# Performance work log

Measured on AMD Instinct MI355X. Metric: run time of the kernel, lower is better.

Reference implementation:

```python
import jax, jax.numpy as jnp
import numpy as np

# Module config (matches init_kwargs)
IC, OC = 8, 16
KH, KW = 3, 3
H, W = 32, 32
PAD, STRIDE = 1, 1
PH, PW = H + 2 * PAD, W + 2 * PAD          # padded input dims: 34x34
OH = (PH - KH) // STRIDE + 1                # 32
OW = (PW - KW) // STRIDE + 1                # 32
B = 64                                       # batch of flattened ciphertext images


def _build_toeplitz(kernel: np.ndarray) -> np.ndarray:
    """approximate_toeplitz_multiple_channels: dense [OC*OH*OW, IC*PH*PW] matrix
    such that T @ vec(padded_x) == vec(conv2d(x, kernel))."""
    T = np.zeros((OC * OH * OW, IC * PH * PW), dtype=np.float32)
    oh, ow = np.meshgrid(np.arange(OH), np.arange(OW), indexing="ij")
    oh, ow = oh.ravel(), ow.ravel()
    for oc in range(OC):
        rows = (oc * OH + oh) * OW + ow
        for ic in range(IC):
            for kh in range(KH):
                for kw in range(KW):
                    cols = (ic * PH + oh * STRIDE + kh) * PW + (ow * STRIDE + kw)
                    T[rows, cols] = kernel[oc, ic, kh, kw]
    return T


def _build_pad_mat() -> np.ndarray:
    """create_padding_transformation_matrix: [IC*PH*PW, IC*H*W] 0/1 matrix that
    zero-pads the flattened image (homomorphic padding as a matmul)."""
    P = np.zeros((IC * PH * PW, IC * H * W), dtype=np.float32)
    ic, h, w = np.meshgrid(np.arange(IC), np.arange(H), np.arange(W), indexing="ij")
    rows = (ic * PH + h + PAD) * PW + (w + PAD)
    cols = (ic * H + h) * W + w
    P[rows.ravel(), cols.ravel()] = 1.0
    return P


def setup_inputs() -> dict:
    rng = np.random.default_rng(0)
    kernel = rng.standard_normal((OC, IC, KH, KW)).astype(np.float32)
    weight = jnp.asarray(_build_toeplitz(kernel))                 # [OC*OH*OW, IC*PH*PW]
    bias = jnp.asarray(
        np.repeat(rng.standard_normal(OC).astype(np.float32), OH * OW)
    )                                                             # [OC*OH*OW]
    pad_mat = jnp.asarray(_build_pad_mat())                       # [IC*PH*PW, IC*H*W]
    key = jax.random.key(0)
    enc_x = jax.random.normal(key, (B, IC * H * W), dtype=jnp.float32)
    return {"enc_x": enc_x, "weight": weight, "bias": bias, "pad_mat": pad_mat}


def reference(enc_x, weight, bias, pad_mat):
    # Homomorphic conv as plaintext-equivalent math:
    # 1) pad via transformation matrix, 2) Toeplitz matmul, 3) add repeated bias.
    x_padded = enc_x @ pad_mat.T            # [B, IC*PH*PW]
    return x_padded @ weight.T + bias       # [B, OC*OH*OW]
```

## Files before the change

### kernel.cpp

```cpp
#include <hip/hip_runtime.h>

#define IC    8
#define OC    16
#define H     32
#define W     32
#define PH    34
#define PW    34
#define OH    32
#define OW    32
#define BATCH 64
#define WCOLS (IC * PH * PW)
#define XSTR  35
#define PLANE (PH * XSTR)
#define HALO  134

__global__ __launch_bounds__(256, 2) void conv_toeplitz_kernel(
    const float* __restrict__ x,
    const float* __restrict__ weight,
    const float* __restrict__ bias,
    float* __restrict__ out)
{
    __shared__ float wk[2][IC * 9];
    __shared__ float xs[IC * PLANE];

    const int tid = threadIdx.x;
    const int blk = blockIdx.x;
    const int b   = blk >> 3;
    const int oc0 = (blk & 7) << 1;

    if (tid < 144) {
        const int os = tid / 72;
        const int k  = tid - os * 72;
        const int ic = k / 9;
        const int r  = k - ic * 9;
        const int kh = r / 3;
        const int kw = r - kh * 3;
        wk[os][k] = weight[(size_t)((oc0 + os) * OH * OW) * WCOLS
                           + (ic * PH + kh) * PW + kw];
    }

    for (int i = tid; i < IC * HALO; i += 256) {
        const int plane = i / HALO;
        const int r     = i - plane * HALO;
        int row, col;
        if (r < 35)       { row = 0;          col = r;        }
        else if (r < 70)  { row = 33;         col = r - 35;   }
        else if (r < 102) { row = r - 70 + 1; col = 0;        }
        else              { row = r - 102 + 1; col = 33;      }
        xs[plane * PLANE + row * XSTR + col] = 0.0f;
    }

    const float4* xg = (const float4*)(x + (size_t)b * (IC * H * W));
    #pragma unroll
    for (int i = 0; i < 8; ++i) {
        const int k   = tid + i * 256;
        const float4 v = xg[k];
        const int ic  = k >> 8;
        const int rem = k & 255;
        const int h   = rem >> 3;
        const int w4  = (rem & 7) << 2;
        float* dst = &xs[ic * PLANE + (h + 1) * XSTR + (w4 + 1)];
        dst[0] = v.x; dst[1] = v.y; dst[2] = v.z; dst[3] = v.w;
    }
    __syncthreads();

    float wreg[2][IC * 9];
    #pragma unroll
    for (int o = 0; o < 2; ++o)
        #pragma unroll
        for (int k = 0; k < IC * 9; ++k)
            wreg[o][k] = wk[o][k];

    const int oh   = tid >> 3;
    const int ow0  = (tid & 7) << 2;
    const int oidx = oh * OW + ow0;

    const float4 b0 = *(const float4*)(bias + oc0 * OH * OW + oidx);
    const float4 b1 = *(const float4*)(bias + (oc0 + 1) * OH * OW + oidx);
    float a00 = b0.x, a01 = b0.y, a02 = b0.z, a03 = b0.w;
    float a10 = b1.x, a11 = b1.y, a12 = b1.z, a13 = b1.w;

    #pragma unroll
    for (int ic = 0; ic < IC; ++ic) {
        #pragma unroll
        for (int kh = 0; kh < 3; ++kh) {
            const float* row = &xs[ic * PLANE + (oh + kh) * XSTR + ow0];
            const float v0 = row[0], v1 = row[1], v2 = row[2];
            const float v3 = row[3], v4 = row[4], v5 = row[5];
            const float w00 = wreg[0][ic * 9 + kh * 3];
            const float w01 = wreg[0][ic * 9 + kh * 3 + 1];
            const float w02 = wreg[0][ic * 9 + kh * 3 + 2];
            const float w10 = wreg[1][ic * 9 + kh * 3];
            const float w11 = wreg[1][ic * 9 + kh * 3 + 1];
            const float w12 = wreg[1][ic * 9 + kh * 3 + 2];
            a00 += v0 * w00 + v1 * w01 + v2 * w02;
            a01 += v1 * w00 + v2 * w01 + v3 * w02;
            a02 += v2 * w00 + v3 * w01 + v4 * w02;
            a03 += v3 * w00 + v4 * w01 + v5 * w02;
            a10 += v0 * w10 + v1 * w11 + v2 * w12;
            a11 += v1 * w10 + v2 * w11 + v3 * w12;
            a12 += v2 * w10 + v3 * w11 + v4 * w12;
            a13 += v3 * w10 + v4 * w11 + v5 * w12;
        }
    }

    float* o0 = out + (size_t)(b * OC + oc0) * (OH * OW) + oidx;
    *(float4*)o0 = make_float4(a00, a01, a02, a03);
    float* o1 = o0 + OH * OW;
    *(float4*)o1 = make_float4(a10, a11, a12, a13);
}

extern "C" void kernel_launch(void* const* d_in, const int* in_sizes, int n_in,
                              void* d_out, int out_size, void* d_ws, size_t ws_size,
                              hipStream_t stream) {
    const float* x      = (const float*)d_in[0];
    const float* weight = (const float*)d_in[1];
    const float* bias   = (const float*)d_in[2];
    float* out = (float*)d_out;

    conv_toeplitz_kernel<<<dim3(BATCH * (OC / 2)), dim3(256), 0, stream>>>(x, weight, bias, out);
}
```

Before: 10.94 us.

## Pad shared tile to 16B-aligned stride and vectorize halo staging and reads

Changes the shared-memory input tile stride from 35 to 36 floats so rows are 16-byte aligned. The tile is now filled with aligned float4 stores that include the zero halo, instead of scalar stores plus a separate halo loop. The inner loop reads each row with a float4 plus float2 load and loads weights per input channel as float4 from a repacked layout rather than keeping all weights in registers. This aims to cut LDS instruction count and register pressure, at the cost of unaligned scalar global loads when building the shifted groups.

```diff
diff --git a/kernel.cpp b/kernel.cpp
--- a/kernel.cpp
+++ b/kernel.cpp
@@ -5,22 +5,20 @@
 #define H     32
 #define W     32
 #define PH    34
-#define PW    34
-#define OH    32
-#define OW    32
 #define BATCH 64
-#define WCOLS (IC * PH * PW)
-#define XSTR  35
+#define WCOLS 9248
+#define XSTR  36
 #define PLANE (PH * XSTR)
-#define HALO  134
+#define NDATA 2304
+#define NGRP  2448
 
-__global__ __launch_bounds__(256, 2) void conv_toeplitz_kernel(
+__global__ __launch_bounds__(256, 2) void conv_pair_v5_kernel(
     const float* __restrict__ x,
     const float* __restrict__ weight,
     const float* __restrict__ bias,
     float* __restrict__ out)
 {
-    __shared__ float wk[2][IC * 9];
+    __shared__ float wk[16 * 12];
     __shared__ float xs[IC * PLANE];
 
     const int tid = threadIdx.x;
@@ -35,79 +33,92 @@
         const int r  = k - ic * 9;
         const int kh = r / 3;
         const int kw = r - kh * 3;
-        wk[os][k] = weight[(size_t)((oc0 + os) * OH * OW) * WCOLS
-                           + (ic * PH + kh) * PW + kw];
+        wk[(ic * 2 + os) * 12 + r] =
+            weight[(size_t)((oc0 + os) << 10) * WCOLS + (ic * PH + kh) * PH + kw];
     }
 
-    for (int i = tid; i < IC * HALO; i += 256) {
-        const int plane = i / HALO;
-        const int r     = i - plane * HALO;
-        int row, col;
-        if (r < 35)       { row = 0;          col = r;        }
-        else if (r < 70)  { row = 33;         col = r - 35;   }
-        else if (r < 102) { row = r - 70 + 1; col = 0;        }
-        else              { row = r - 102 + 1; col = 33;      }
-        xs[plane * PLANE + row * XSTR + col] = 0.0f;
+    const float* xb = x + ((size_t)b << 13);
+    float4 vals[10];
+    int    dsta[10];
+    #pragma unroll
+    for (int it = 0; it < 10; ++it) {
+        const int idx = tid + (it << 8);
+        float4 v = make_float4(0.f, 0.f, 0.f, 0.f);
+        int ic, row, g;
+        if (idx < NDATA) {
+            ic = idx / 288;
+            const int rem = idx - ic * 288;
+            row = rem / 9 + 1;
+            g   = rem - (row - 1) * 9;
+            const int o = ((ic << 5) + (row - 1)) << 5;
+            if (g == 0)      v = make_float4(0.f, xb[o], xb[o + 1], xb[o + 2]);
+            else if (g == 8) v = make_float4(xb[o + 31], 0.f, 0.f, 0.f);
+            else {
+                const float* p = xb + o + (g << 2) - 1;
+                v = make_float4(p[0], p[1], p[2], p[3]);
+            }
+        } else {
+            const int z = idx - NDATA;
+            ic = z / 18;
+            const int zz = z - ic * 18;
+            row = (zz >= 9) ? 33 : 0;
+            g   = (zz >= 9) ? zz - 9 : zz;
+        }
+        vals[it] = v;
+        dsta[it] = ic * PLANE + row * XSTR + (g << 2);
     }
-
-    const float4* xg = (const float4*)(x + (size_t)b * (IC * H * W));
     #pragma unroll
-    for (int i = 0; i < 8; ++i) {
-        const int k   = tid + i * 256;
-        const float4 v = xg[k];
-        const int ic  = k >> 8;
-        const int rem = k & 255;
-        const int h   = rem >> 3;
-        const int w4  = (rem & 7) << 2;
-        float* dst = &xs[ic * PLANE + (h + 1) * XSTR + (w4 + 1)];
-        dst[0] = v.x; dst[1] = v.y; dst[2] = v.z; dst[3] = v.w;
+    for (int it = 0; it < 10; ++it) {
+        const int idx = tid + (it << 8);
+        if (idx < NGRP) *(float4*)&xs[dsta[it]] = vals[it];
     }
     __syncthreads();
 
-    float wreg[2][IC * 9];
-    #pragma unroll
-    for (int o = 0; o < 2; ++o)
-        #pragma unroll
-        for (int k = 0; k < IC * 9; ++k)
-            wreg[o][k] = wk[o][k];
-
     const int oh   = tid >> 3;
     const int ow0  = (tid & 7) << 2;
-    const int oidx = oh * OW + ow0;
+    const int oidx = (oh << 5) + ow0;
 
-    const float4 b0 = *(const float4*)(bias + oc0 * OH * OW + oidx);
-    const float4 b1 = *(const float4*)(bias + (oc0 + 1) * OH * OW + oidx);
+    const float4 b0 = *(const float4*)(bias + (oc0 << 10) + oidx);
+    const float4 b1 = *(const float4*)(bias + ((oc0 + 1) << 10) + oidx);
     float a00 = b0.x, a01 = b0.y, a02 = b0.z, a03 = b0.w;
     float a10 = b1.x, a11 = b1.y, a12 = b1.z, a13 = b1.w;
 
     #pragma unroll
     for (int ic = 0; ic < IC; ++ic) {
+        float w[2][12];
+        #pragma unroll
+        for (int os = 0; os < 2; ++os)
+            #pragma unroll
+            for (int i = 0; i < 3; ++i)
+                *(float4*)&w[os][i * 4] = *(const float4*)&wk[(ic * 2 + os) * 12 + i * 4];
+
         #pragma unroll
         for (int kh = 0; kh < 3; ++kh) {
-            const float* row = &xs[ic * PLANE + (oh + kh) * XSTR + ow0];
-            const float v0 = row[0], v1 = row[1], v2 = row[2];
-            const float v3 = row[3], v4 = row[4], v5 = row[5];
-            const float w00 = wreg[0][ic * 9 + kh * 3];
-            const float w01 = wreg[0][ic * 9 + kh * 3 + 1];
-            const float w02 = wreg[0][ic * 9 + kh * 3 + 2];
-            const float w10 = wreg[1][ic * 9 + kh * 3];
-            const float w11 = wreg[1][ic * 9 + kh * 3 + 1];
-            const float w12 = wreg[1][ic * 9 + kh * 3 + 2];
-            a00 += v0 * w00 + v1 * w01 + v2 * w02;
-            a01 += v1 * w00 + v2 * w01 + v3 * w02;
-            a02 += v2 * w00 + v3 * w01 + v4 * w02;
-            a03 += v3 * w00 + v4 * w01 + v5 * w02;
-            a10 += v0 * w10 + v1 * w11 + v2 * w12;
-            a11 += v1 * w10 + v2 * w11 + v3 * w12;
-            a12 += v2 * w10 + v3 * w11 + v4 * w12;
-            a13 += v3 * w10 + v4 * w11 + v5 * w12;
+            const float* rp = &xs[ic * PLANE + (oh + kh) * XSTR + ow0];
+            const float4 va = *(const float4*)rp;
+            const float2 vb = *(const float2*)(rp + 4);
+            const float v0 = va.x, v1 = va.y, v2 = va.z, v3 = va.w;
+            const float v4 = vb.x, v5 = vb.y;
+            {
+                const float w0 = w[0][kh * 3], w1 = w[0][kh * 3 + 1], w2 = w[0][kh * 3 + 2];
+                a00 += v0 * w0 + v1 * w1 + v2 * w2;
+                a01 += v1 * w0 + v2 * w1 + v3 * w2;
+                a02 += v2 * w0 + v3 * w1 + v4 * w2;
+                a03 += v3 * w0 + v4 * w1 + v5 * w2;
+            }
+            {
+                const float w0 = w[1][kh * 3], w1 = w[1][kh * 3 + 1], w2 = w[1][kh * 3 + 2];
+                a10 += v0 * w0 + v1 * w1 + v2 * w2;
+                a11 += v1 * w0 + v2 * w1 + v3 * w2;
+                a12 += v2 * w0 + v3 * w1 + v4 * w2;
+                a13 += v3 * w0 + v4 * w1 + v5 * w2;
+            }
         }
     }
 
-    float* o0 = out + (size_t)(b * OC + oc0) * (OH * OW) + oidx;
+    float* o0 = out + (size_t)(((b << 4) + oc0) << 10) + oidx;
     *(float4*)o0 = make_float4(a00, a01, a02, a03);
-    float* o1 = o0 + OH * OW;
-    *(float4*)o1 = make_float4(a10, a11, a12, a13);
+    *(float4*)(o0 + 1024) = make_float4(a10, a11, a12, a13);
 }
 
 extern "C" void kernel_launch(void* const* d_in, const int* in_sizes, int n_in,
@@ -118,5 +129,5 @@
     const float* bias   = (const float*)d_in[2];
     float* out = (float*)d_out;
 
-    conv_toeplitz_kernel<<<dim3(BATCH * (OC / 2)), dim3(256), 0, stream>>>(x, weight, bias, out);
+    conv_pair_v5_kernel<<<dim3(BATCH * 8), dim3(256), 0, stream>>>(x, weight, bias, out);
 }
```

New measurement: 13.65 us. +24.7%, slower.
